# Performance work log

Measured on AMD Instinct MI355X. Metric: run time of the kernel, lower is better.

Reference implementation:

```python
import jax, jax.numpy as jnp
import numpy as np

N_NODES = 100000
N_EDGES = 3200000
F_IN = 512
F_OUT = 256


def setup_inputs() -> dict:
    key = jax.random.key(0)
    k1, k2, k3, k4, k5 = jax.random.split(key, 5)
    x = jax.random.normal(k1, (N_NODES, F_IN), dtype=jnp.float32)
    adj_rows = jax.random.randint(k2, (N_EDGES,), 0, N_NODES, dtype=jnp.int32)
    adj_cols = jax.random.randint(k3, (N_EDGES,), 0, N_NODES, dtype=jnp.int32)
    adj_vals = jax.random.uniform(k4, (N_EDGES,), dtype=jnp.float32)
    # glorot-uniform weight as in glorot_init
    init_range = np.sqrt(6.0 / (F_IN + F_OUT))
    weight = jax.random.uniform(k5, (F_IN, F_OUT), dtype=jnp.float32,
                                minval=-init_range, maxval=init_range)
    return {"x": x, "adj_rows": adj_rows, "adj_cols": adj_cols,
            "adj_vals": adj_vals, "weight": weight}


def reference(x, adj_rows, adj_cols, adj_vals, adj_rows_dummy=None, **_):
    raise NotImplementedError  # replaced below


def reference(x, adj_rows, adj_cols, adj_vals, weight):
    # dropout p=0.0 -> identity
    h = jnp.matmul(x, weight)                      # [N, Fout] dense GEMM
    # SpMM: out[r] = sum_e vals[e] * h[cols[e]] for rows[e]==r
    msgs = adj_vals[:, None] * h[adj_cols]         # [E, Fout] gather + scale
    out = jax.ops.segment_sum(msgs, adj_rows, num_segments=x.shape[0])
    return jax.nn.relu(out)
```

## Files before the change

kernel.cpp:

```cpp
#include <hip/hip_runtime.h>

#define F_IN 512
#define F_OUT 256
#define BM 128
#define BN 256
#define BK 64

#define RB_BITS 6
#define RPB 64
#define NBUCK 2048
#define NSUB 8
#define CAP_SUB 512
#define SLOTS_PER_BUCKET (NSUB * CAP_SUB)
#define LDSSORT 3072
#define CSTR 16

typedef __attribute__((ext_vector_type(8))) short bf16x8;
typedef __attribute__((ext_vector_type(4))) float f32x4;
typedef __attribute__((ext_vector_type(4))) int i32x4;
typedef __attribute__((ext_vector_type(2))) int i32x2;

__device__ __forceinline__ ushort f2bf(float f) {
    union { float f; unsigned u; } c{f};
    unsigned r = (c.u + 0x7FFF + ((c.u >> 16) & 1)) >> 16;
    return (ushort)r;
}
__device__ __forceinline__ float bf2f(ushort b) {
    union { unsigned u; float f; } c{(unsigned)b << 16};
    return c.f;
}

__global__ __launch_bounds__(256) void conv_w(const float* __restrict__ w,
                                              ushort* __restrict__ wt) {
    int idx = blockIdx.x * 256 + threadIdx.x;
    int k = idx & (F_IN - 1);
    int n = idx >> 9;
    wt[(size_t)n * F_IN + k] = f2bf(w[(size_t)k * F_OUT + n]);
}

__global__ __launch_bounds__(512) void gemm_place(const float* __restrict__ x,
                                                  const ushort* __restrict__ wt,
                                                  ushort* __restrict__ h,
                                                  int n_nodes,
                                                  const int* __restrict__ rows,
                                                  const int* __restrict__ cols,
                                                  const float* __restrict__ vals,
                                                  int* __restrict__ bcur,
                                                  int2* __restrict__ edges,
                                                  int n_edges,
                                                  int ngemm) {
    __shared__ short As[BM * BK];
    __shared__ short Bs[BN * BK];
    const int bid = blockIdx.x;
    const int t = threadIdx.x;

    const bool is_gemm = (bid % 3 == 0) && (bid / 3 < ngemm);
    if (!is_gemm) {
        const int place_id = (bid < 3 * ngemm) ? (bid - bid / 3 - 1) : (bid - ngemm);
        const int sub = bid & (NSUB - 1);
        int base = (place_id * 512 + t) * 4;
        if (base >= n_edges) return;
        if (base + 3 < n_edges) {
            i32x4 r4 = __builtin_nontemporal_load(reinterpret_cast<const i32x4*>(rows + base));
            i32x4 c4 = __builtin_nontemporal_load(reinterpret_cast<const i32x4*>(cols + base));
            f32x4 v4 = __builtin_nontemporal_load(reinterpret_cast<const f32x4*>(vals + base));
#pragma unroll
            for (int j = 0; j < 4; ++j) {
                int r = r4[j];
                int bs = (r >> RB_BITS) * NSUB + sub;
                int p = atomicAdd(&bcur[bs * CSTR], 1);
                if (p < CAP_SUB)
                    edges[(size_t)bs * CAP_SUB + p] =
                        make_int2(((r & (RPB - 1)) << 17) | c4[j], __float_as_int(v4[j]));
            }
        } else {
            for (int j = 0; j < 4 && base + j < n_edges; ++j) {
                int r = rows[base + j];
                int bs = (r >> RB_BITS) * NSUB + sub;
                int p = atomicAdd(&bcur[bs * CSTR], 1);
                if (p < CAP_SUB)
                    edges[(size_t)bs * CAP_SUB + p] =
                        make_int2(((r & (RPB - 1)) << 17) | cols[base + j],
                                  __float_as_int(vals[base + j]));
            }
        }
        return;
    }

    const int gb = bid / 3;
    const int lane = t & 63;
    const int w = t >> 6;
    const int wm = w >> 2;
    const int wn = w & 3;
    const int row0 = gb * BM;

    f32x4 acc[4][4] = {};

    const int arow = t >> 2;
    const int akq  = (t & 3) << 4;
    const bool avalid = (row0 + arow) < n_nodes;
    const float* xsrc = x + (size_t)(row0 + arow) * F_IN + akq;

    const int lrow = lane & 15;
    const int koff = (lane >> 4) << 3;

    f32x4 fA[4];
    bf16x8 fB[4];

    {
        if (avalid) {
            const f32x4* s4 = reinterpret_cast<const f32x4*>(xsrc);
            fA[0] = __builtin_nontemporal_load(s4 + 0);
            fA[1] = __builtin_nontemporal_load(s4 + 1);
            fA[2] = __builtin_nontemporal_load(s4 + 2);
            fA[3] = __builtin_nontemporal_load(s4 + 3);
        } else {
            fA[0] = 0.f; fA[1] = 0.f; fA[2] = 0.f; fA[3] = 0.f;
        }
#pragma unroll
        for (int p = 0; p < 4; ++p) {
            int cid = p * 512 + t;
            int n = cid >> 3;
            int j = cid & 7;
            fB[p] = *reinterpret_cast<const bf16x8*>(wt + (size_t)n * F_IN + j * 8);
        }
    }

    for (int k0 = 0; k0 < F_IN; k0 += BK) {
#pragma unroll
        for (int q = 0; q < 2; ++q) {
            bf16x8 v;
#pragma unroll
            for (int j = 0; j < 8; ++j) v[j] = (short)f2bf(fA[q * 2 + (j >> 2)][j & 3]);
            int kk = akq + q * 8;
            int idx = arow * BK + (kk ^ ((arow & 7) << 3));
            *reinterpret_cast<bf16x8*>(&As[idx]) = v;
        }
#pragma unroll
        for (int p = 0; p < 4; ++p) {
            int cid = p * 512 + t;
            int n = cid >> 3;
            int j = cid & 7;
            int idx = n * BK + ((j * 8) ^ ((n & 7) << 3));
            *reinterpret_cast<bf16x8*>(&Bs[idx]) = fB[p];
        }
        __syncthreads();

        if (k0 + BK < F_IN) {
            if (avalid) {
                const f32x4* s4 = reinterpret_cast<const f32x4*>(xsrc + k0 + BK);
                fA[0] = __builtin_nontemporal_load(s4 + 0);
                fA[1] = __builtin_nontemporal_load(s4 + 1);
                fA[2] = __builtin_nontemporal_load(s4 + 2);
                fA[3] = __builtin_nontemporal_load(s4 + 3);
            }
#pragma unroll
            for (int p = 0; p < 4; ++p) {
                int cid = p * 512 + t;
                int n = cid >> 3;
                int j = cid & 7;
                fB[p] = *reinterpret_cast<const bf16x8*>(wt + (size_t)n * F_IN + k0 + BK + j * 8);
            }
        }

#pragma unroll
        for (int kk = 0; kk < BK; kk += 32) {
            bf16x8 a[4], b[4];
#pragma unroll
            for (int m = 0; m < 4; ++m) {
                int r = wm * 64 + m * 16 + lrow;
                int idx = r * BK + ((kk + koff) ^ ((r & 7) << 3));
                a[m] = *reinterpret_cast<const bf16x8*>(&As[idx]);
            }
#pragma unroll
            for (int n = 0; n < 4; ++n) {
                int r = wn * 64 + n * 16 + lrow;
                int idx = r * BK + ((kk + koff) ^ ((r & 7) << 3));
                b[n] = *reinterpret_cast<const bf16x8*>(&Bs[idx]);
            }
#pragma unroll
            for (int m = 0; m < 4; ++m)
#pragma unroll
                for (int n = 0; n < 4; ++n)
                    acc[m][n] = __builtin_amdgcn_mfma_f32_16x16x32_bf16(a[m], b[n], acc[m][n], 0, 0, 0);
        }
        __syncthreads();
    }

    const int rbase_ = (lane >> 4) << 2;
#pragma unroll
    for (int m = 0; m < 4; ++m) {
#pragma unroll
        for (int r = 0; r < 4; ++r) {
            int orow = row0 + wm * 64 + m * 16 + rbase_ + r;
            if (orow < n_nodes) {
                ushort* dst = h + (size_t)orow * F_OUT + wn * 64 + lrow;
#pragma unroll
                for (int n = 0; n < 4; ++n) dst[n * 16] = f2bf(acc[m][n][r]);
            }
        }
    }
}

struct EB { i32x4 e0, e1, e2, e3; };
struct GB { ushort4 g0, g1, g2, g3, g4, g5, g6, g7; };

__device__ __forceinline__ void load_eb_lds(EB& e, const int2* __restrict__ sl, int i) {
    const i32x4* p = reinterpret_cast<const i32x4*>(sl + i);
    e.e0 = p[0]; e.e1 = p[1]; e.e2 = p[2]; e.e3 = p[3];
}
__device__ __forceinline__ void issue_gb(GB& g, const EB& e, const ushort* __restrict__ hf) {
    g.g0 = *reinterpret_cast<const ushort4*>(hf + (size_t)e.e0[0] * F_OUT);
    g.g1 = *reinterpret_cast<const ushort4*>(hf + (size_t)e.e0[2] * F_OUT);
    g.g2 = *reinterpret_cast<const ushort4*>(hf + (size_t)e.e1[0] * F_OUT);
    g.g3 = *reinterpret_cast<const ushort4*>(hf + (size_t)e.e1[2] * F_OUT);
    g.g4 = *reinterpret_cast<const ushort4*>(hf + (size_t)e.e2[0] * F_OUT);
    g.g5 = *reinterpret_cast<const ushort4*>(hf + (size_t)e.e2[2] * F_OUT);
    g.g6 = *reinterpret_cast<const ushort4*>(hf + (size_t)e.e3[0] * F_OUT);
    g.g7 = *reinterpret_cast<const ushort4*>(hf + (size_t)e.e3[2] * F_OUT);
}
__device__ __forceinline__ void fma1(float* acc, float v, ushort4 g) {
    acc[0] = fmaf(v, bf2f(g.x), acc[0]);
    acc[1] = fmaf(v, bf2f(g.y), acc[1]);
    acc[2] = fmaf(v, bf2f(g.z), acc[2]);
    acc[3] = fmaf(v, bf2f(g.w), acc[3]);
}
__device__ __forceinline__ void fma_gb(float* acc, const EB& e, const GB& g) {
    fma1(acc, __int_as_float(e.e0[1]), g.g0);
    fma1(acc, __int_as_float(e.e0[3]), g.g1);
    fma1(acc, __int_as_float(e.e1[1]), g.g2);
    fma1(acc, __int_as_float(e.e1[3]), g.g3);
    fma1(acc, __int_as_float(e.e2[1]), g.g4);
    fma1(acc, __int_as_float(e.e2[3]), g.g5);
    fma1(acc, __int_as_float(e.e3[1]), g.g6);
    fma1(acc, __int_as_float(e.e3[3]), g.g7);
}

__global__ __launch_bounds__(256) void sort_spmm(const int* __restrict__ bcur,
                                                 const int2* __restrict__ edges,
                                                 const ushort* __restrict__ h,
                                                 float* __restrict__ out,
                                                 int n_nodes) {
    __shared__ int2 sorted[LDSSORT];
    __shared__ int cnt[RPB];
    __shared__ int rbase[RPB];
    __shared__ int rcnt[RPB];
    __shared__ int lcur[RPB];
    const int b = blockIdx.x;
    const int t = threadIdx.x;
    const int wv = t >> 6;
    const int lane = t & 63;
    const size_t bbase = (size_t)b * SLOTS_PER_BUCKET;

    if (t < RPB) cnt[t] = 0;
    __syncthreads();

#pragma unroll
    for (int s = 0; s < NSUB; ++s) {
        int ns = bcur[(b * NSUB + s) * CSTR];
        if (ns > CAP_SUB) ns = CAP_SUB;
        for (int i = t; i < ns; i += 256) {
            i32x2 ev = __builtin_nontemporal_load(
                reinterpret_cast<const i32x2*>(edges + bbase + (size_t)s * CAP_SUB + i));
            atomicAdd(&cnt[ev[0] >> 17], 1);
        }
    }
    __syncthreads();

    int c = (t < RPB) ? cnt[t] : 0;
    int padded = (c + 7) & ~7;
    int x = padded;
#pragma unroll
    for (int d = 1; d < 64; d <<= 1) {
        int y = __shfl_up(x, d, 64);
        if (lane >= d) x += y;
    }
    if (t < RPB) {
        int base = x - padded;
        if (base > LDSSORT) base = LDSSORT;
        int end = base + padded;
        if (end > LDSSORT) end = LDSSORT;
        rbase[t] = base;
        rcnt[t] = (end - base) & ~7;
        lcur[t] = base;
        for (int j = c; j < padded; ++j) {
            int p = base + j;
            if (p < LDSSORT) sorted[p] = make_int2(0, 0);
        }
    }
    __syncthreads();

#pragma unroll
    for (int s = 0; s < NSUB; ++s) {
        int ns = bcur[(b * NSUB + s) * CSTR];
        if (ns > CAP_SUB) ns = CAP_SUB;
        for (int i = t; i < ns; i += 256) {
            i32x2 ev = __builtin_nontemporal_load(
                reinterpret_cast<const i32x2*>(edges + bbase + (size_t)s * CAP_SUB + i));
            int pos = atomicAdd(&lcur[ev[0] >> 17], 1);
            if (pos < LDSSORT) sorted[pos] = make_int2(ev[0] & 0x1FFFF, ev[1]);
        }
    }
    __syncthreads();

    const int row0 = b * RPB;
    const ushort* hf = h + lane * 4;
    for (int row = wv; row < RPB; row += 4) {
        const int beg = rbase[row];
        const int nb = rcnt[row] >> 3;
        float acc[4] = {0.f, 0.f, 0.f, 0.f};

        if (nb > 0) {
            EB ea, eb_;
            GB ga, gb;
            load_eb_lds(ea, sorted, beg);
            issue_gb(ga, ea, hf);
            int bi = 1;
            for (; bi + 1 < nb; bi += 2) {
                load_eb_lds(eb_, sorted, beg + bi * 8);
                issue_gb(gb, eb_, hf);
                fma_gb(acc, ea, ga);
                load_eb_lds(ea, sorted, beg + (bi + 1) * 8);
                issue_gb(ga, ea, hf);
                fma_gb(acc, eb_, gb);
            }
            if (bi < nb) {
                load_eb_lds(eb_, sorted, beg + bi * 8);
                issue_gb(gb, eb_, hf);
                fma_gb(acc, ea, ga);
                fma_gb(acc, eb_, gb);
            } else {
                fma_gb(acc, ea, ga);
            }
        }

        int gr = row0 + row;
        if (gr < n_nodes) {
            f32x4 o;
            o[0] = fmaxf(acc[0], 0.f);
            o[1] = fmaxf(acc[1], 0.f);
            o[2] = fmaxf(acc[2], 0.f);
            o[3] = fmaxf(acc[3], 0.f);
            __builtin_nontemporal_store(
                o, reinterpret_cast<f32x4*>(out + (size_t)gr * F_OUT + lane * 4));
        }
    }
}

static inline size_t align_up(size_t v, size_t a) { return (v + a - 1) & ~(a - 1); }

extern "C" void kernel_launch(void* const* d_in, const int* in_sizes, int n_in,
                              void* d_out, int out_size, void* d_ws, size_t ws_size,
                              hipStream_t stream) {
    const float* x    = (const float*)d_in[0];
    const int*   rows = (const int*)d_in[1];
    const int*   cols = (const int*)d_in[2];
    const float* vals = (const float*)d_in[3];
    const float* w    = (const float*)d_in[4];
    float* out = (float*)d_out;

    const int n_nodes = in_sizes[0] / F_IN;
    const int n_edges = in_sizes[1];
    const int nbuck_used = (n_nodes + RPB - 1) >> RB_BITS;

    char* ws = (char*)d_ws;
    size_t off = 0;
    ushort* h   = (ushort*)(ws + off); off = align_up(off + (size_t)n_nodes * F_OUT * 2, 256);
    ushort* wt  = (ushort*)(ws + off); off = align_up(off + (size_t)F_OUT * F_IN * 2, 256);
    int2* edges = (int2*)(ws + off);   off = align_up(off + (size_t)NBUCK * SLOTS_PER_BUCKET * 8, 256);
    int* bcur   = (int*)(ws + off);    off = align_up(off + (size_t)NBUCK * NSUB * CSTR * 4, 256);
    (void)ws_size;

    conv_w<<<(F_IN * F_OUT) / 256, 256, 0, stream>>>(w, wt);
    hipMemsetAsync(bcur, 0, (size_t)NBUCK * NSUB * CSTR * 4, stream);

    const int ngemm  = (n_nodes + BM - 1) / BM;
    const int nplace = (n_edges + 2047) / 2048;
    gemm_place<<<ngemm + nplace, 512, 0, stream>>>(x, wt, h, n_nodes,
                                                   rows, cols, vals, bcur, edges,
                                                   n_edges, ngemm);

    sort_spmm<<<nbuck_used, 256, 0, stream>>>(bcur, edges, h, out, n_nodes);
}
```

Before: 434.0 us.

## Precompute per-row edge counts in placement pass and widen SpMM blocks to 512 threads

The placement phase now also does a global atomicAdd per edge into a per-row counts array. This lets the sort_spmm kernel drop its first pass over the bucketed edges, which only counted edges per row with LDS atomics. sort_spmm is also launched with 512 threads, and each of its 8 waves handles 8 consecutive rows. The cost is 3.2M extra global atomics and a larger memset. If a bucket overflows CAP_SUB, the global counts can disagree with the edges actually stored, leaving zero-padded or stale slots.

```diff
diff --git a/kernel.cpp b/kernel.cpp
--- a/kernel.cpp
+++ b/kernel.cpp
@@ -46,6 +46,7 @@
                                                   const int* __restrict__ cols,
                                                   const float* __restrict__ vals,
                                                   int* __restrict__ bcur,
+                                                  int* __restrict__ counts,
                                                   int2* __restrict__ edges,
                                                   int n_edges,
                                                   int ngemm) {
@@ -69,6 +70,7 @@
                 int r = r4[j];
                 int bs = (r >> RB_BITS) * NSUB + sub;
                 int p = atomicAdd(&bcur[bs * CSTR], 1);
+                atomicAdd(&counts[r], 1);
                 if (p < CAP_SUB)
                     edges[(size_t)bs * CAP_SUB + p] =
                         make_int2(((r & (RPB - 1)) << 17) | c4[j], __float_as_int(v4[j]));
@@ -78,6 +80,7 @@
                 int r = rows[base + j];
                 int bs = (r >> RB_BITS) * NSUB + sub;
                 int p = atomicAdd(&bcur[bs * CSTR], 1);
+                atomicAdd(&counts[r], 1);
                 if (p < CAP_SUB)
                     edges[(size_t)bs * CAP_SUB + p] =
                         make_int2(((r & (RPB - 1)) << 17) | cols[base + j],
@@ -236,13 +239,13 @@
     fma1(acc, __int_as_float(e.e3[3]), g.g7);
 }
 
-__global__ __launch_bounds__(256) void sort_spmm(const int* __restrict__ bcur,
+__global__ __launch_bounds__(512) void sort_spmm(const int* __restrict__ counts,
+                                                 const int* __restrict__ bcur,
                                                  const int2* __restrict__ edges,
                                                  const ushort* __restrict__ h,
                                                  float* __restrict__ out,
                                                  int n_nodes) {
     __shared__ int2 sorted[LDSSORT];
-    __shared__ int cnt[RPB];
     __shared__ int rbase[RPB];
     __shared__ int rcnt[RPB];
     __shared__ int lcur[RPB];
@@ -251,23 +254,13 @@
     const int wv = t >> 6;
     const int lane = t & 63;
     const size_t bbase = (size_t)b * SLOTS_PER_BUCKET;
-
-    if (t < RPB) cnt[t] = 0;
-    __syncthreads();
-
-#pragma unroll
-    for (int s = 0; s < NSUB; ++s) {
-        int ns = bcur[(b * NSUB + s) * CSTR];
-        if (ns > CAP_SUB) ns = CAP_SUB;
-        for (int i = t; i < ns; i += 256) {
-            i32x2 ev = __builtin_nontemporal_load(
-                reinterpret_cast<const i32x2*>(edges + bbase + (size_t)s * CAP_SUB + i));
-            atomicAdd(&cnt[ev[0] >> 17], 1);
-        }
-    }
-    __syncthreads();
-
-    int c = (t < RPB) ? cnt[t] : 0;
+    const int row0 = b * RPB;
+
+    int c = 0;
+    if (t < RPB) {
+        int gr = row0 + t;
+        c = (gr < n_nodes) ? counts[gr] : 0;
+    }
     int padded = (c + 7) & ~7;
     int x = padded;
 #pragma unroll
@@ -294,7 +287,7 @@
     for (int s = 0; s < NSUB; ++s) {
         int ns = bcur[(b * NSUB + s) * CSTR];
         if (ns > CAP_SUB) ns = CAP_SUB;
-        for (int i = t; i < ns; i += 256) {
+        for (int i = t; i < ns; i += 512) {
             i32x2 ev = __builtin_nontemporal_load(
                 reinterpret_cast<const i32x2*>(edges + bbase + (size_t)s * CAP_SUB + i));
             int pos = atomicAdd(&lcur[ev[0] >> 17], 1);
@@ -303,9 +296,10 @@
     }
     __syncthreads();
 
-    const int row0 = b * RPB;
     const ushort* hf = h + lane * 4;
-    for (int row = wv; row < RPB; row += 4) {
+#pragma unroll 1
+    for (int rr = 0; rr < 8; ++rr) {
+        const int row = wv * 8 + rr;
         const int beg = rbase[row];
         const int nb = rcnt[row] >> 3;
         float acc[4] = {0.f, 0.f, 0.f, 0.f};
@@ -368,17 +362,20 @@
     ushort* h   = (ushort*)(ws + off); off = align_up(off + (size_t)n_nodes * F_OUT * 2, 256);
     ushort* wt  = (ushort*)(ws + off); off = align_up(off + (size_t)F_OUT * F_IN * 2, 256);
     int2* edges = (int2*)(ws + off);   off = align_up(off + (size_t)NBUCK * SLOTS_PER_BUCKET * 8, 256);
+    size_t zero_beg = off;
+    int* counts = (int*)(ws + off);    off = align_up(off + (size_t)n_nodes * 4, 256);
     int* bcur   = (int*)(ws + off);    off = align_up(off + (size_t)NBUCK * NSUB * CSTR * 4, 256);
+    size_t zero_span = off - zero_beg;
     (void)ws_size;
 
     conv_w<<<(F_IN * F_OUT) / 256, 256, 0, stream>>>(w, wt);
-    hipMemsetAsync(bcur, 0, (size_t)NBUCK * NSUB * CSTR * 4, stream);
+    hipMemsetAsync(ws + zero_beg, 0, zero_span, stream);
 
     const int ngemm  = (n_nodes + BM - 1) / BM;
     const int nplace = (n_edges + 2047) / 2048;
     gemm_place<<<ngemm + nplace, 512, 0, stream>>>(x, wt, h, n_nodes,
-                                                   rows, cols, vals, bcur, edges,
-                                                   n_edges, ngemm);
-
-    sort_spmm<<<nbuck_used, 256, 0, stream>>>(bcur, edges, h, out, n_nodes);
-}
+                                                   rows, cols, vals, bcur, counts,
+                                                   edges, n_edges, ngemm);
+
+    sort_spmm<<<nbuck_used, 512, 0, stream>>>(counts, bcur, edges, h, out, n_nodes);
+}
```

Result: slower. 520.4 us (+19.9%).
